# Performance work log

Hardware: AMD Instinct MI355X
Metric: run time of the kernel (lower is better)

The kernel has to match this reference:

```python
import jax, jax.numpy as jnp
import numpy as np

B = 4096
IN_F = 4096
OUT_F = 4096
IN_Q = IN_F // 4
OUT_Q = OUT_F // 4


def setup_inputs() -> dict:
    key = jax.random.key(0)
    ks = jax.random.split(key, 9)
    scale = 1.0 / np.sqrt(IN_Q)
    inp = {"x": jax.random.normal(ks[0], (B, IN_F), dtype=jnp.float32)}
    for i, name in enumerate(["rr", "ri", "rj", "rk"]):
        inp[f"W_{name}"] = jax.random.uniform(ks[1 + i], (OUT_Q, IN_Q), dtype=jnp.float32, minval=-scale, maxval=scale)
        inp[f"b_{name}"] = jax.random.uniform(ks[5 + i], (OUT_Q,), dtype=jnp.float32, minval=-scale, maxval=scale)
    return inp


def reference(x, W_rr, W_ri, W_rj, W_rk, b_rr, b_ri, b_rj, b_rk):
    b = x.shape[0]
    # split into quaternion components: chunks c in {r,i,j,k}
    xs = x.reshape(b, 4, IN_Q)                       # [B, 4, IN_Q]
    W = jnp.stack([W_rr, W_ri, W_rj, W_rk])          # [4(lin), OUT_Q, IN_Q]
    bias = jnp.stack([b_rr, b_ri, b_rj, b_rk])       # [4(lin), OUT_Q]
    # all 16 linear applications in one batched GEMM: Y[b,c,q,:] = lin_q(x_c)
    Y = jnp.einsum('bci,qoi->bcqo', xs, W) + bias    # [B, 4, 4, OUT_Q]
    out_r = Y[:, 0, 0] - Y[:, 1, 1] - Y[:, 2, 2] - Y[:, 3, 3]
    out_i = Y[:, 0, 1] + Y[:, 1, 0] + Y[:, 2, 3] - Y[:, 3, 2]
    out_j = Y[:, 0, 2] - Y[:, 1, 3] + Y[:, 2, 0] + Y[:, 3, 1]
    out_k = Y[:, 0, 3] + Y[:, 1, 2] - Y[:, 2, 1] + Y[:, 3, 0]
    out = jnp.stack([out_r, out_i, out_j, out_k], axis=1)  # [B, 4, OUT_Q]
    return out.reshape(b, -1)                        # [B, OUT_F]
```

## Files before the change

kernel.cpp:

```cpp
#include <hip/hip_runtime.h>
#include <cstdint>
#include <cstddef>

#define MDIM 4096
#define NDIM 4096
#define KDIM 4096

typedef _Float16 half8   __attribute__((ext_vector_type(8)));
typedef float    floatx4 __attribute__((ext_vector_type(4)));

__device__ __constant__ int   d_qtab[16] = {0,1,2,3,  1,0,3,2,  2,3,0,1,  3,2,1,0};
__device__ __constant__ float d_stab[16] = {1.f,-1.f,-1.f,-1.f,
                                            1.f, 1.f, 1.f,-1.f,
                                            1.f,-1.f, 1.f, 1.f,
                                            1.f, 1.f,-1.f, 1.f};

__global__ void prepass_kernel(const float* __restrict__ x,
                               const float* __restrict__ W0, const float* __restrict__ W1,
                               const float* __restrict__ W2, const float* __restrict__ W3,
                               _Float16* __restrict__ xh, _Float16* __restrict__ Wh) {
    int b = blockIdx.x;
    if (b < 8192) {
        int idx = b * 256 + threadIdx.x;
        const float4* src = (const float4*)x + (size_t)idx * 2;
        float4 a = src[0], v = src[1];
        half8 h = {(_Float16)a.x, (_Float16)a.y, (_Float16)a.z, (_Float16)a.w,
                   (_Float16)v.x, (_Float16)v.y, (_Float16)v.z, (_Float16)v.w};
        ((half8*)xh)[idx] = h;
    } else {
        int idx = (b - 8192) * 256 + threadIdx.x;
        int e = idx << 3;
        int m = e >> 20;
        int off = e & ((1 << 20) - 1);
        const float* Ws[4] = {W0, W1, W2, W3};
        const float* src = Ws[m] + off;
        float4 a = *(const float4*)src;
        float4 v = *(const float4*)(src + 4);
        half8 h = {(_Float16)a.x, (_Float16)a.y, (_Float16)a.z, (_Float16)a.w,
                   (_Float16)v.x, (_Float16)v.y, (_Float16)v.z, (_Float16)v.w};
        *(half8*)(Wh + ((size_t)m << 20) + off) = h;
    }
}


__device__ __forceinline__ void gload_lds16(const _Float16* g, _Float16* l) {
    __builtin_amdgcn_global_load_lds(
        (const __attribute__((address_space(1))) unsigned int*)g,
        (__attribute__((address_space(3))) unsigned int*)l,
        16, 0, 0);
}

#define BAR __builtin_amdgcn_s_barrier()
#define WAITLGKM do { asm volatile("s_waitcnt lgkmcnt(0)" ::: "memory"); \
                      __builtin_amdgcn_sched_barrier(0); } while (0)
#define WAITVM(N) asm volatile("s_waitcnt vmcnt(" #N ")" ::: "memory")

#define STA(g, tt, buf) { \
    const _Float16* _s = Abase + (size_t)((g) * 64) * KDIM + (tt) * 64; \
    _Float16* _d = AsSt + (buf) * 16384 + (g) * 8192; \
    gload_lds16(_s, _d); \
    gload_lds16(_s + (size_t)128 * KDIM, _d + 4096); }

#define STB(h, tt, buf) { \
    const int _sg = (tt) >> 4; \
    const _Float16* _s = Bbase + ((size_t)(comp ^ _sg) << 20) \
                       + (size_t)((h) * 128) * 1024 + ((tt) & 15) * 64; \
    _Float16* _d = BsSt + (buf) * 16384 + (h) * 8192; \
    gload_lds16(_s, _d); \
    gload_lds16(_s + 64 * 1024, _d + 4096); }

#define RDA(g, SL) { \
    const _Float16* _p = Acur + (g) * 8192 + arow + (SL); \
    af[0] = *(const half8*)(_p); \
    af[1] = *(const half8*)(_p + 1024); \
    af[2] = *(const half8*)(_p + 2048); \
    af[3] = *(const half8*)(_p + 3072); }

#define RDB(BQ, SL) { \
    const _Float16* _p = Bcur + bnh * 8192 + brow + (SL); \
    BQ[0] = *(const half8*)(_p); \
    BQ[1] = *(const half8*)(_p + 1024); \
    BQ[2] = *(const half8*)(_p + 2048); \
    BQ[3] = *(const half8*)(_p + 3072); \
    if (bneg) { BQ[0] = -BQ[0]; BQ[1] = -BQ[1]; BQ[2] = -BQ[2]; BQ[3] = -BQ[3]; } }

#define MFMA16(IB, BQ) \
    _Pragma("unroll") \
    for (int _i = 0; _i < 4; _i++) \
      _Pragma("unroll") \
      for (int _j = 0; _j < 4; _j++) \
        acc[(IB) + _i][_j] = __builtin_amdgcn_mfma_f32_16x16x32_f16( \
            af[_i], BQ[_j], acc[(IB) + _i][_j], 0, 0, 0);

__global__ __launch_bounds__(512, 2) void gemm_kernel(
        const _Float16* __restrict__ A,
        const _Float16* __restrict__ Wh,
        const float* __restrict__ b0, const float* __restrict__ b1,
        const float* __restrict__ b2, const float* __restrict__ b3,
        float* __restrict__ C) {
    __shared__ _Float16 lds[65536];
    _Float16* As = lds;
    _Float16* Bs = lds + 32768;

    const int tid  = threadIdx.x;
    const int lane = tid & 63;
    const int wave = tid >> 6;
    const int wmh  = wave >> 2;
    const int wn   = (wave & 3) * 64;
    const int bnh  = wn >> 7;
    const int broff = (wn & 64) * 64;

    const int wg = ((blockIdx.x & 7) << 5) | (blockIdx.x >> 3);
    const int bm = wg >> 4, bn = wg & 15;
    const int m0 = bm << 8;
    const int n0 = bn << 8;
    const int comp = bn >> 2;
    const int n0q  = n0 & 1023;

    const int lrow = tid >> 3;
    const int gch  = (tid & 7) ^ (lrow & 7);
    const _Float16* Abase = A  + (size_t)(m0  + lrow) * KDIM + gch * 8;
    const _Float16* Bbase = Wh + (size_t)(n0q + lrow) * 1024 + gch * 8;
    _Float16* AsSt = As + tid * 8;
    _Float16* BsSt = Bs + tid * 8;

    const int fr  = lane & 15;
    const int qf  = lane >> 4;
    const int fsw = fr & 7;
    const int sl0 = ((0 + qf) ^ fsw) * 8;
    const int sl1 = ((4 + qf) ^ fsw) * 8;
    const int arow = wmh * 4096 + fr * 64;
    const int brow = broff + fr * 64;

    const int negseg = (comp == 0) ? 0 : (comp == 1) ? 3 : (comp == 2) ? 1 : 2;
    const float flip = (comp == 0) ? -1.f : 1.f;

    floatx4 acc[8][4];
#pragma unroll
    for (int i = 0; i < 8; i++)
#pragma unroll
        for (int j = 0; j < 4; j++)
            acc[i][j] = (floatx4){0.f, 0.f, 0.f, 0.f};

    STA(0, 0, 0); STB(0, 0, 0); STB(1, 0, 0); STA(1, 0, 0);
    STA(0, 1, 1); STB(0, 1, 1);
    WAITVM(6);
    BAR;

    for (int tt = 0; tt < 64; ++tt) {
        const int cur = tt & 1, nxt = cur ^ 1;
        const bool bneg = ((tt >> 4) == negseg);
        const _Float16* Acur = As + cur * 16384;
        const _Float16* Bcur = Bs + cur * 16384;
        const int t1 = (tt >= 63) ? 63 : tt + 1;
        const int t2 = (tt >= 62) ? 63 : tt + 2;
        half8 af[4], bf0[4], bf1[4];

        RDA(0, sl0); RDB(bf0, sl0);
        STB(1, t1, nxt);
        WAITLGKM;
        __builtin_amdgcn_s_setprio(1);
        MFMA16(0, bf0);
        __builtin_amdgcn_s_setprio(0);
        BAR;

        RDA(0, sl1); RDB(bf1, sl1);
        STA(1, t1, nxt);
        WAITLGKM;
        __builtin_amdgcn_s_setprio(1);
        MFMA16(0, bf1);
        __builtin_amdgcn_s_setprio(0);
        WAITVM(8);
        BAR;

        RDA(1, sl0);
        STA(0, t2, cur);
        WAITLGKM;
        __builtin_amdgcn_s_setprio(1);
        MFMA16(4, bf0);
        __builtin_amdgcn_s_setprio(0);
        BAR;

        RDA(1, sl1);
        STB(0, t2, cur);
        WAITLGKM;
        __builtin_amdgcn_s_setprio(1);
        MFMA16(4, bf1);
        __builtin_amdgcn_s_setprio(0);
        WAITVM(6);
        BAR;
    }

    WAITVM(0);

    const int col   = lane & 15;
    const int rquad = (lane >> 4) * 4;
    const int wm    = wmh * 128;
    const float* bsp[4] = {b0, b1, b2, b3};
#pragma unroll
    for (int j = 0; j < 4; j++) {
        const int gn = n0 + wn + j * 16 + col;
        const int o  = gn & 1023;
        float bv = 0.f;
#pragma unroll
        for (int c = 0; c < 4; c++)
            bv += d_stab[comp * 4 + c] * bsp[comp ^ c][o];
#pragma unroll
        for (int i = 0; i < 8; i++) {
            const int gmb = m0 + wm + i * 16 + rquad;
#pragma unroll
            for (int r = 0; r < 4; r++)
                C[(size_t)(gmb + r) * NDIM + gn] = flip * acc[i][j][r] + bv;
        }
    }
}

__global__ void fallback_kernel(const float* __restrict__ x,
                                const float* __restrict__ W0, const float* __restrict__ W1,
                                const float* __restrict__ W2, const float* __restrict__ W3,
                                const float* __restrict__ b0, const float* __restrict__ b1,
                                const float* __restrict__ b2, const float* __restrict__ b3,
                                float* __restrict__ out) {
    int idx = blockIdx.x * 256 + threadIdx.x;
    int m = idx >> 12, n = idx & 4095;
    int comp = n >> 10, o = n & 1023;
    const float* Ws[4] = {W0, W1, W2, W3};
    const float* bs[4] = {b0, b1, b2, b3};
    float acc = 0.f;
    for (int c = 0; c < 4; c++) {
        int t = comp * 4 + c;
        const float* wr = Ws[d_qtab[t]] + (size_t)o * 1024;
        const float* xr = x + (size_t)m * 4096 + c * 1024;
        float s = d_stab[t];
        float dot = 0.f;
        for (int i = 0; i < 1024; i += 4) {
            float4 wv = *(const float4*)(wr + i);
            float4 xv = *(const float4*)(xr + i);
            dot += wv.x * xv.x + wv.y * xv.y + wv.z * xv.z + wv.w * xv.w;
        }
        acc += s * dot + s * bs[d_qtab[t]][o];
    }
    out[idx] = acc;
}

extern "C" void kernel_launch(void* const* d_in, const int* in_sizes, int n_in,
                              void* d_out, int out_size, void* d_ws, size_t ws_size,
                              hipStream_t stream) {
    const float* x = (const float*)d_in[0];
    const float* W[4];
    const float* b[4];
    int wi = 0, bi = 0;
    for (int i = 1; i < n_in && i < 9; i++) {
        if (in_sizes[i] > 4096) { if (wi < 4) W[wi++] = (const float*)d_in[i]; }
        else                    { if (bi < 4) b[bi++] = (const float*)d_in[i]; }
    }
    float* out = (float*)d_out;

    const size_t xh_elems = (size_t)MDIM * KDIM;
    const size_t wh_elems = (size_t)4 * 1024 * 1024;
    const size_t needed = (xh_elems + wh_elems) * 2;

    if (ws_size < needed) {
        fallback_kernel<<<(MDIM * NDIM) / 256, 256, 0, stream>>>(
            x, W[0], W[1], W[2], W[3], b[0], b[1], b[2], b[3], out);
        return;
    }

    _Float16* xh = (_Float16*)d_ws;
    _Float16* Wh = xh + xh_elems;

    prepass_kernel<<<8192 + 2048, 256, 0, stream>>>(x, W[0], W[1], W[2], W[3], xh, Wh);
    gemm_kernel<<<(MDIM / 256) * (NDIM / 256), 512, 0, stream>>>(
        xh, Wh, b[0], b[1], b[2], b[3], out);
}
```

Baseline: 256.4 us.

## Software-pipeline LDS fragment reads one phase ahead of MFMA blocks

Double-buffers the A/B register fragments so that LDS reads for the next MFMA phase are issued before the current MFMA block, replacing the explicit lgkmcnt(0) waits with plain scheduling barriers. The next tile's first fragments are prefetched from the other LDS buffer at the end of each iteration, and the vmcnt waits are moved to earlier phases so that data is ready. The goal is to hide LDS read latency behind matrix-core work. In exchange it raises register pressure under a 2-waves-per-SIMD launch bound, and it depends on the compiler inserting correct waitcnts for the LDS reads.

```diff
diff --git a/kernel.cpp b/kernel.cpp
--- a/kernel.cpp
+++ b/kernel.cpp
@@ -51,8 +51,7 @@
 }
 
 #define BAR __builtin_amdgcn_s_barrier()
-#define WAITLGKM do { asm volatile("s_waitcnt lgkmcnt(0)" ::: "memory"); \
-                      __builtin_amdgcn_sched_barrier(0); } while (0)
+#define SCHEDB __builtin_amdgcn_sched_barrier(0)
 #define WAITVM(N) asm volatile("s_waitcnt vmcnt(" #N ")" ::: "memory")
 
 #define STA(g, tt, buf) { \
@@ -69,28 +68,28 @@
     gload_lds16(_s, _d); \
     gload_lds16(_s + 64 * 1024, _d + 4096); }
 
-#define RDA(g, SL) { \
-    const _Float16* _p = Acur + (g) * 8192 + arow + (SL); \
-    af[0] = *(const half8*)(_p); \
-    af[1] = *(const half8*)(_p + 1024); \
-    af[2] = *(const half8*)(_p + 2048); \
-    af[3] = *(const half8*)(_p + 3072); }
-
-#define RDB(BQ, SL) { \
-    const _Float16* _p = Bcur + bnh * 8192 + brow + (SL); \
+#define RDA(AF, BASE, g, SL) { \
+    const _Float16* _p = (BASE) + (g) * 8192 + arow + (SL); \
+    AF[0] = *(const half8*)(_p); \
+    AF[1] = *(const half8*)(_p + 1024); \
+    AF[2] = *(const half8*)(_p + 2048); \
+    AF[3] = *(const half8*)(_p + 3072); }
+
+#define RDB(BQ, BASE, SL, NEG) { \
+    const _Float16* _p = (BASE) + bnh * 8192 + brow + (SL); \
     BQ[0] = *(const half8*)(_p); \
     BQ[1] = *(const half8*)(_p + 1024); \
     BQ[2] = *(const half8*)(_p + 2048); \
     BQ[3] = *(const half8*)(_p + 3072); \
-    if (bneg) { BQ[0] = -BQ[0]; BQ[1] = -BQ[1]; BQ[2] = -BQ[2]; BQ[3] = -BQ[3]; } }
-
-#define MFMA16(IB, BQ) \
+    if (NEG) { BQ[0] = -BQ[0]; BQ[1] = -BQ[1]; BQ[2] = -BQ[2]; BQ[3] = -BQ[3]; } }
+
+#define MFMA16(IB, AF, BQ) \
     _Pragma("unroll") \
     for (int _i = 0; _i < 4; _i++) \
       _Pragma("unroll") \
       for (int _j = 0; _j < 4; _j++) \
         acc[(IB) + _i][_j] = __builtin_amdgcn_mfma_f32_16x16x32_f16( \
-            af[_i], BQ[_j], acc[(IB) + _i][_j], 0, 0, 0);
+            AF[_i], BQ[_j], acc[(IB) + _i][_j], 0, 0, 0);
 
 __global__ __launch_bounds__(512, 2) void gemm_kernel(
         const _Float16* __restrict__ A,
@@ -142,52 +141,57 @@
         for (int j = 0; j < 4; j++)
             acc[i][j] = (floatx4){0.f, 0.f, 0.f, 0.f};
 
+    half8 afP[4], afQ[4], bf0[4], bf1[4];
+
     STA(0, 0, 0); STB(0, 0, 0); STB(1, 0, 0); STA(1, 0, 0);
     STA(0, 1, 1); STB(0, 1, 1);
     WAITVM(6);
     BAR;
+    RDA(afP, As, 0, sl0); RDB(bf0, Bs, sl0, (0 == negseg));
 
     for (int tt = 0; tt < 64; ++tt) {
         const int cur = tt & 1, nxt = cur ^ 1;
-        const bool bneg = ((tt >> 4) == negseg);
+        const bool bneg  = ((tt >> 4) == negseg);
         const _Float16* Acur = As + cur * 16384;
         const _Float16* Bcur = Bs + cur * 16384;
+        const _Float16* Anxt = As + nxt * 16384;
+        const _Float16* Bnxt = Bs + nxt * 16384;
         const int t1 = (tt >= 63) ? 63 : tt + 1;
         const int t2 = (tt >= 62) ? 63 : tt + 2;
-        half8 af[4], bf0[4], bf1[4];
-
-        RDA(0, sl0); RDB(bf0, sl0);
+        const bool bneg1 = ((t1 >> 4) == negseg);
+
+        RDA(afQ, Acur, 0, sl1); RDB(bf1, Bcur, sl1, bneg);
         STB(1, t1, nxt);
-        WAITLGKM;
-        __builtin_amdgcn_s_setprio(1);
-        MFMA16(0, bf0);
-        __builtin_amdgcn_s_setprio(0);
-        BAR;
-
-        RDA(0, sl1); RDB(bf1, sl1);
+        SCHEDB;
+        __builtin_amdgcn_s_setprio(1);
+        MFMA16(0, afP, bf0);
+        __builtin_amdgcn_s_setprio(0);
+        WAITVM(6);
+        BAR;
+
+        RDA(afP, Acur, 1, sl0);
         STA(1, t1, nxt);
-        WAITLGKM;
-        __builtin_amdgcn_s_setprio(1);
-        MFMA16(0, bf1);
-        __builtin_amdgcn_s_setprio(0);
-        WAITVM(8);
-        BAR;
-
-        RDA(1, sl0);
+        SCHEDB;
+        __builtin_amdgcn_s_setprio(1);
+        MFMA16(0, afQ, bf1);
+        __builtin_amdgcn_s_setprio(0);
+        BAR;
+
+        RDA(afQ, Acur, 1, sl1);
         STA(0, t2, cur);
-        WAITLGKM;
-        __builtin_amdgcn_s_setprio(1);
-        MFMA16(4, bf0);
-        __builtin_amdgcn_s_setprio(0);
-        BAR;
-
-        RDA(1, sl1);
+        SCHEDB;
+        __builtin_amdgcn_s_setprio(1);
+        MFMA16(4, afP, bf0);
+        __builtin_amdgcn_s_setprio(0);
+        WAITVM(4);
+        BAR;
+
+        RDA(afP, Anxt, 0, sl0); RDB(bf0, Bnxt, sl0, bneg1);
         STB(0, t2, cur);
-        WAITLGKM;
-        __builtin_amdgcn_s_setprio(1);
-        MFMA16(4, bf1);
-        __builtin_amdgcn_s_setprio(0);
-        WAITVM(6);
+        SCHEDB;
+        __builtin_amdgcn_s_setprio(1);
+        MFMA16(4, afQ, bf1);
+        __builtin_amdgcn_s_setprio(0);
         BAR;
     }
 
```

Measured after the change: 257.1 us (median of 2 runs). Within noise of the previous version (+0.3%).

## Restructure GEMM main loop phases and replace per-fragment B negation with accumulator flips

Applied to the files above, without the earlier changes.

The main loop is reorganized into four phases that each read a full K slice (both sub-slices) of A and half of B, with different global-to-LDS staging order and wait counts. The per-iteration negation of B fragments for the negative segment is replaced by flipping the whole accumulator at segment boundaries, with a final sign applied in the epilogue. This is meant to cut register pressure and VALU work on B fragments and to improve overlap between LDS reads, async loads and MFMA. In exchange it adds more barriers per iteration, and the sign bookkeeping across segments is error-prone.

```diff
diff --git a/kernel.cpp b/kernel.cpp
--- a/kernel.cpp
+++ b/kernel.cpp
@@ -51,9 +51,11 @@
 }
 
 #define BAR __builtin_amdgcn_s_barrier()
-#define WAITLGKM do { asm volatile("s_waitcnt lgkmcnt(0)" ::: "memory"); \
-                      __builtin_amdgcn_sched_barrier(0); } while (0)
+#define SCHEDB __builtin_amdgcn_sched_barrier(0)
 #define WAITVM(N) asm volatile("s_waitcnt vmcnt(" #N ")" ::: "memory")
+#define LGKM8 asm volatile("s_waitcnt lgkmcnt(8)" ::: "memory")
+#define WAITLGKM0 do { asm volatile("s_waitcnt lgkmcnt(0)" ::: "memory"); \
+                       SCHEDB; } while (0)
 
 #define STA(g, tt, buf) { \
     const _Float16* _s = Abase + (size_t)((g) * 64) * KDIM + (tt) * 64; \
@@ -69,28 +71,31 @@
     gload_lds16(_s, _d); \
     gload_lds16(_s + 64 * 1024, _d + 4096); }
 
-#define RDA(g, SL) { \
-    const _Float16* _p = Acur + (g) * 8192 + arow + (SL); \
-    af[0] = *(const half8*)(_p); \
-    af[1] = *(const half8*)(_p + 1024); \
-    af[2] = *(const half8*)(_p + 2048); \
-    af[3] = *(const half8*)(_p + 3072); }
-
-#define RDB(BQ, SL) { \
-    const _Float16* _p = Bcur + bnh * 8192 + brow + (SL); \
-    BQ[0] = *(const half8*)(_p); \
-    BQ[1] = *(const half8*)(_p + 1024); \
-    BQ[2] = *(const half8*)(_p + 2048); \
-    BQ[3] = *(const half8*)(_p + 3072); \
-    if (bneg) { BQ[0] = -BQ[0]; BQ[1] = -BQ[1]; BQ[2] = -BQ[2]; BQ[3] = -BQ[3]; } }
-
-#define MFMA16(IB, BQ) \
+#define RDA2(BASE, g) { \
+    const _Float16* _p = (BASE) + (g) * 8192 + arow; \
+    af[0][0] = *(const half8*)(_p + sl0);        af[0][1] = *(const half8*)(_p + sl1); \
+    af[1][0] = *(const half8*)(_p + 1024 + sl0); af[1][1] = *(const half8*)(_p + 1024 + sl1); \
+    af[2][0] = *(const half8*)(_p + 2048 + sl0); af[2][1] = *(const half8*)(_p + 2048 + sl1); \
+    af[3][0] = *(const half8*)(_p + 3072 + sl0); af[3][1] = *(const half8*)(_p + 3072 + sl1); }
+
+#define RDB2(BASE, jb) { \
+    const _Float16* _p = (BASE) + bnh * 8192 + brow + (jb) * 1024; \
+    bf[0][0] = *(const half8*)(_p + sl0);        bf[0][1] = *(const half8*)(_p + sl1); \
+    bf[1][0] = *(const half8*)(_p + 1024 + sl0); bf[1][1] = *(const half8*)(_p + 1024 + sl1); }
+
+#define MFMAPH(IB, JB) { \
     _Pragma("unroll") \
     for (int _i = 0; _i < 4; _i++) \
       _Pragma("unroll") \
-      for (int _j = 0; _j < 4; _j++) \
-        acc[(IB) + _i][_j] = __builtin_amdgcn_mfma_f32_16x16x32_f16( \
-            af[_i], BQ[_j], acc[(IB) + _i][_j], 0, 0, 0);
+      for (int _j = 0; _j < 2; _j++) \
+        acc[(IB) + _i][(JB) + _j] = __builtin_amdgcn_mfma_f32_16x16x32_f16( \
+            af[_i][0], bf[_j][0], acc[(IB) + _i][(JB) + _j], 0, 0, 0); \
+    _Pragma("unroll") \
+    for (int _i = 0; _i < 4; _i++) \
+      _Pragma("unroll") \
+      for (int _j = 0; _j < 2; _j++) \
+        acc[(IB) + _i][(JB) + _j] = __builtin_amdgcn_mfma_f32_16x16x32_f16( \
+            af[_i][1], bf[_j][1], acc[(IB) + _i][(JB) + _j], 0, 0, 0); }
 
 __global__ __launch_bounds__(512, 2) void gemm_kernel(
         const _Float16* __restrict__ A,
@@ -133,7 +138,9 @@
     const int brow = broff + fr * 64;
 
     const int negseg = (comp == 0) ? 0 : (comp == 1) ? 3 : (comp == 2) ? 1 : 2;
-    const float flip = (comp == 0) ? -1.f : 1.f;
+    const int negFlipA = (negseg == 0) ? 16 : negseg * 16;
+    const int negFlipB = (negseg == 0 || negseg == 3) ? -1 : negseg * 16 + 16;
+    const float esign = (comp <= 1) ? -1.f : 1.f;
 
     floatx4 acc[8][4];
 #pragma unroll
@@ -142,52 +149,62 @@
         for (int j = 0; j < 4; j++)
             acc[i][j] = (floatx4){0.f, 0.f, 0.f, 0.f};
 
-    STA(0, 0, 0); STB(0, 0, 0); STB(1, 0, 0); STA(1, 0, 0);
-    STA(0, 1, 1); STB(0, 1, 1);
-    WAITVM(6);
+    half8 af[4][2], bf[2][2];
+
+    STA(0, 0, 0); STA(1, 0, 0);
+    STB(0, 0, 0); STB(1, 0, 0);
+    STA(0, 1, 1);
+    WAITVM(2);
     BAR;
 
     for (int tt = 0; tt < 64; ++tt) {
         const int cur = tt & 1, nxt = cur ^ 1;
-        const bool bneg = ((tt >> 4) == negseg);
         const _Float16* Acur = As + cur * 16384;
         const _Float16* Bcur = Bs + cur * 16384;
         const int t1 = (tt >= 63) ? 63 : tt + 1;
         const int t2 = (tt >= 62) ? 63 : tt + 2;
-        half8 af[4], bf0[4], bf1[4];
-
-        RDA(0, sl0); RDB(bf0, sl0);
+
+        if (tt == negFlipA || tt == negFlipB) {
+#pragma unroll
+            for (int i = 0; i < 8; i++)
+#pragma unroll
+                for (int j = 0; j < 4; j++)
+                    acc[i][j] = -acc[i][j];
+        }
+
+        RDA2(Acur, 0);
+        RDB2(Bcur, 0);
+        STA(1, t1, nxt);
+        STB(0, t1, nxt);
         STB(1, t1, nxt);
-        WAITLGKM;
-        __builtin_amdgcn_s_setprio(1);
-        MFMA16(0, bf0);
-        __builtin_amdgcn_s_setprio(0);
-        BAR;
-
-        RDA(0, sl1); RDB(bf1, sl1);
-        STA(1, t1, nxt);
-        WAITLGKM;
-        __builtin_amdgcn_s_setprio(1);
-        MFMA16(0, bf1);
-        __builtin_amdgcn_s_setprio(0);
-        WAITVM(8);
-        BAR;
-
-        RDA(1, sl0);
+        LGKM8;
+        BAR; WAITLGKM0;
+        __builtin_amdgcn_s_setprio(1);
+        MFMAPH(0, 0);
+        __builtin_amdgcn_s_setprio(0);
+        BAR;
+
+        RDB2(Bcur, 2);
+        BAR; WAITLGKM0;
+        __builtin_amdgcn_s_setprio(1);
+        MFMAPH(0, 2);
+        __builtin_amdgcn_s_setprio(0);
+        BAR;
+
+        RDA2(Acur, 1);
         STA(0, t2, cur);
-        WAITLGKM;
-        __builtin_amdgcn_s_setprio(1);
-        MFMA16(4, bf0);
-        __builtin_amdgcn_s_setprio(0);
-        BAR;
-
-        RDA(1, sl1);
-        STB(0, t2, cur);
-        WAITLGKM;
-        __builtin_amdgcn_s_setprio(1);
-        MFMA16(4, bf1);
-        __builtin_amdgcn_s_setprio(0);
-        WAITVM(6);
+        BAR; WAITLGKM0;
+        __builtin_amdgcn_s_setprio(1);
+        MFMAPH(4, 2);
+        __builtin_amdgcn_s_setprio(0);
+        BAR;
+
+        RDB2(Bcur, 0);
+        BAR; WAITLGKM0;
+        __builtin_amdgcn_s_setprio(1);
+        MFMAPH(4, 0);
+        __builtin_amdgcn_s_setprio(0);
+        WAITVM(2);
         BAR;
     }
 
@@ -210,7 +227,7 @@
             const int gmb = m0 + wm + i * 16 + rquad;
 #pragma unroll
             for (int r = 0; r < 4; r++)
-                C[(size_t)(gmb + r) * NDIM + gn] = flip * acc[i][j][r] + bv;
+                C[(size_t)(gmb + r) * NDIM + gn] = esign * acc[i][j][r] + bv;
         }
     }
 }
```

After: 268.1 us. +4.5%, slower.
